# Kernel tuning notes

Measured on AMD Instinct MI355X. Metric: run time of the kernel, lower is better.

Reference implementation:

```python
import jax, jax.numpy as jnp
import numpy as np

NUM_NODES = 100000
NUM_HYPEREDGES = 100000
NNZ = 1600000
K = 64
LAMBDA_ORTHO = 0.1


def setup_inputs() -> dict:
    key = jax.random.key(0)
    k1, k2, k3 = jax.random.split(key, 3)
    Z = jax.random.normal(k1, (NUM_NODES, K), dtype=jnp.float32)
    hyperedge_index = jax.random.randint(k2, (2, NNZ), 0, NUM_HYPEREDGES, dtype=jnp.int64)
    hyperedge_weight = jax.random.uniform(k3, (NUM_HYPEREDGES,), dtype=jnp.float32)
    return {
        "Z": Z,
        "hyperedge_index": hyperedge_index,
        "num_nodes": NUM_NODES,
        "hyperedge_weight": hyperedge_weight,
    }


def reference(Z, hyperedge_index, num_nodes, hyperedge_weight):
    E = hyperedge_weight.shape[0]  # num_hyperedges (static)
    node_idx = hyperedge_index[0]
    edge_idx = hyperedge_index[1]

    # Node degree Dv = sum of incident hyperedge weights; clamp zeros to 1.
    w_exp = hyperedge_weight[edge_idx]                                  # [nnz]
    Dv = jax.ops.segment_sum(w_exp, node_idx, num_segments=num_nodes)   # [N]
    Dv = jnp.where(Dv == 0, jnp.ones_like(Dv), Dv)
    Y = Z * (Dv ** -0.5)[:, None]                                       # [N, k]

    # Hyperedge cardinality De (clamped) and raw counts n_e.
    ones = jnp.ones_like(edge_idx, dtype=Z.dtype)
    n_e = jax.ops.segment_sum(ones, edge_idx, num_segments=E)           # [E]
    De = jnp.where(n_e == 0, jnp.ones_like(n_e), n_e)

    # Closed form for the per-edge pairwise-distance loop:
    # 0.5 * sum_{i,j in e} |y_i - y_j|^2 = n_e * sum_i |y_i|^2 - |sum_i y_i|^2
    Yg = Y[node_idx]                                                    # [nnz, k]
    sum_e = jax.ops.segment_sum(Yg, edge_idx, num_segments=E)           # [E, k]
    ss_e = jax.ops.segment_sum(jnp.sum(Yg * Yg, axis=-1), edge_idx, num_segments=E)  # [E]
    per_edge = n_e * ss_e - jnp.sum(sum_e * sum_e, axis=-1)             # [E]
    loss = jnp.sum(hyperedge_weight / De * per_edge)

    # Orthogonality penalty: ||Y^T Y - I||_F
    k = Z.shape[1]
    G = Y.T @ Y - jnp.eye(k, dtype=Z.dtype)
    ortho_loss = jnp.sqrt(jnp.sum(G * G))

    return loss + LAMBDA_ORTHO * ortho_loss
```

## Files before the change

kernel.cpp:

```cpp
#include <hip/hip_runtime.h>
#include <math.h>

#define NNODES 100000
#define NEDGES 100000
#define NNZV   1600000
#define KDIM   64
#define LAMBDA 0.1f

#define NB    782
#define BSH   7
#define BMASK 127
#define CAP   3072
#define A0B   256
#define A0T   1024
#define CHUNK 6250
#define GMB   512

#define OFF_G       0
#define OFF_PART    16384
#define OFF_ZN      19712
#define OFF_GC1     23040
#define OFF_GC2     26368
#define OFF_S1      29696
#define OFF_S2      9638912
#define OFF_YQ      19248128

#if defined(__has_builtin)
#if __has_builtin(__builtin_amdgcn_cvt_f32_fp8)
#define HAS_CVT_FP8 1
#endif
#if __has_builtin(__builtin_amdgcn_cvt_pk_fp8_f32)
#define HAS_PK_FP8 1
#endif
#if __has_builtin(__builtin_amdgcn_cvt_pk_f32_fp8)
#define HAS_PK_F32_FP8 1
typedef float f32x2 __attribute__((ext_vector_type(2)));
#endif
#endif

__device__ __forceinline__ int load_node(const unsigned* idx, int i, bool i64) {
    return (int)(i64 ? idx[2 * i] : idx[i]);
}
__device__ __forceinline__ int load_edge(const unsigned* idx, int i, bool i64) {
    return (int)(i64 ? idx[2 * (NNZV + i)] : idx[NNZV + i]);
}

__device__ __forceinline__ unsigned char enc_fp8(float x) {
    unsigned u = __float_as_uint(x);
    unsigned s = (u >> 31) << 7;
    unsigned mag = u & 0x7FFFFFFFu;
    if (mag >= 0x43E00000u) return (unsigned char)(s | 0x7Eu);
    if (mag < 0x3C800000u) {
        float a = __uint_as_float(mag);
        int m = (int)rintf(a * 512.0f);
        if (m >= 8) return (unsigned char)(s | 0x08u);
        return (unsigned char)(s | (unsigned)m);
    }
    unsigned lsb = (mag >> 20) & 1u;
    mag += 0x0007FFFFu + lsb;
    unsigned e = (mag >> 23) - 120u;
    return (unsigned char)(s | (e << 3) | ((mag >> 20) & 7u));
}

__device__ __forceinline__ unsigned pack_fp8x4(float y0, float y1, float y2, float y3) {
#ifdef HAS_PK_FP8
    int q = 0;
    q = __builtin_amdgcn_cvt_pk_fp8_f32(y0, y1, q, false);
    q = __builtin_amdgcn_cvt_pk_fp8_f32(y2, y3, q, true);
    return (unsigned)q;
#else
    return (unsigned)enc_fp8(y0) | ((unsigned)enc_fp8(y1) << 8) |
           ((unsigned)enc_fp8(y2) << 16) | ((unsigned)enc_fp8(y3) << 24);
#endif
}

template <int SEL>
__device__ __forceinline__ float dec_fp8(unsigned v) {
#ifdef HAS_CVT_FP8
    return __builtin_amdgcn_cvt_f32_fp8(v, SEL);
#else
    unsigned b = (v >> (8 * SEL)) & 0xFFu;
    unsigned e = (b >> 3) & 15u, m = b & 7u;
    float f = e ? __uint_as_float(((e + 120u) << 23) | (m << 20))
                : (float)m * 0.001953125f;
    return (b & 128u) ? -f : f;
#endif
}

__device__ __forceinline__ void dec4_fp8(unsigned v, float& a0, float& a1,
                                         float& a2, float& a3) {
#ifdef HAS_PK_F32_FP8
    f32x2 lo = __builtin_amdgcn_cvt_pk_f32_fp8((int)v, false);
    f32x2 hi = __builtin_amdgcn_cvt_pk_f32_fp8((int)v, true);
    a0 = lo.x; a1 = lo.y; a2 = hi.x; a3 = hi.y;
#else
    a0 = dec_fp8<0>(v); a1 = dec_fp8<1>(v);
    a2 = dec_fp8<2>(v); a3 = dec_fp8<3>(v);
#endif
}

__global__ void init_kernel(unsigned* __restrict__ gcur1,
                            unsigned* __restrict__ gcur2,
                            float* __restrict__ G) {
    int i = blockIdx.x * 256 + threadIdx.x;
    if (i < NB) {
        gcur1[i] = (unsigned)i * CAP;
        gcur2[i] = (unsigned)i * CAP;
    }
    if (i < KDIM * KDIM) G[i] = 0.0f;
}

__global__ __launch_bounds__(A0T) void sort_kernel(const unsigned* __restrict__ idx,
                                                   unsigned* __restrict__ gcur1,
                                                   unsigned* __restrict__ gcur2,
                                                   unsigned* __restrict__ S1,
                                                   unsigned* __restrict__ S2) {
    __shared__ unsigned stage[CHUNK];
    __shared__ unsigned lhist[NB], lcur[NB], gbase[NB];
    __shared__ unsigned wsum[16], fred[16];
    int which = blockIdx.x >> 8, chunk = blockIdx.x & (A0B - 1);
    int t = threadIdx.x, wave = t >> 6, lane = t & 63;

    unsigned hv = idx[2 * t + 1];
#pragma unroll
    for (int off = 32; off; off >>= 1) hv |= __shfl_xor(hv, off);
    if (lane == 0) fred[wave] = hv;
    for (int j = t; j < NB; j += A0T) lhist[j] = 0u;
    __syncthreads();
    unsigned o = 0;
#pragma unroll
    for (int k = 0; k < 16; ++k) o |= fred[k];
    bool i64 = (o == 0u);

    int base = chunk * CHUNK;
    if (which == 0) {
        for (int i = base + t; i < base + CHUNK; i += A0T)
            atomicAdd(&lhist[load_edge(idx, i, i64) >> BSH], 1u);
    } else {
        for (int i = base + t; i < base + CHUNK; i += A0T)
            atomicAdd(&lhist[load_node(idx, i, i64) >> BSH], 1u);
    }
    __syncthreads();

    unsigned v = (t < NB) ? lhist[t] : 0u;
    unsigned x = v;
#pragma unroll
    for (int off = 1; off < 64; off <<= 1) {
        unsigned y = __shfl_up(x, off);
        if (lane >= off) x += y;
    }
    if (lane == 63) wsum[wave] = x;
    __syncthreads();
    if (t < 16) {
        unsigned a = wsum[t], y = a;
#pragma unroll
        for (int off = 1; off < 16; off <<= 1) {
            unsigned z = __shfl_up(y, off);
            if (t >= off) y += z;
        }
        wsum[t] = y - a;
    }
    __syncthreads();
    if (t < NB) lcur[t] = wsum[wave] + x - v;
    __syncthreads();

    for (int i = base + t; i < base + CHUNK; i += A0T) {
        int node = load_node(idx, i, i64);
        int edge = load_edge(idx, i, i64);
        unsigned key, val;
        if (which == 0) {
            key = (unsigned)edge >> BSH;
            val = (unsigned)node | ((unsigned)(edge & BMASK) << 17);
        } else {
            key = (unsigned)node >> BSH;
            val = (unsigned)edge | ((unsigned)(node & BMASK) << 17);
        }
        unsigned p = atomicAdd(&lcur[key], 1u);
        stage[p] = val;
    }
    __syncthreads();

    unsigned* gcur = which ? gcur2 : gcur1;
    if (t < NB) {
        unsigned c = lhist[t];
        gbase[t] = c ? atomicAdd(&gcur[t], c) : 0u;
    }
    __syncthreads();

    unsigned* S = which ? S2 : S1;
    int li = lane & 7;
    for (int bb = wave * 8 + (lane >> 3); bb < NB; bb += 128) {
        unsigned c = lhist[bb];
        unsigned st = lcur[bb] - c;
        unsigned g = gbase[bb];
        for (unsigned m = li; m < c; m += 8) S[g + m] = stage[st + m];
    }
}

__global__ __launch_bounds__(256) void dvyq_kernel(const unsigned* __restrict__ S2,
                                                   const unsigned* __restrict__ gcur2,
                                                   const float* __restrict__ w,
                                                   const float* __restrict__ Z,
                                                   unsigned* __restrict__ Yq32,
                                                   float* __restrict__ ZN) {
    __shared__ float accd[128];
    __shared__ float red[256];
    int t = threadIdx.x, b = blockIdx.x;
    if (t < 128) accd[t] = 0.0f;
    __syncthreads();
    unsigned cnt = gcur2[b] - (unsigned)b * CAP;
    const unsigned* src = S2 + (size_t)b * CAP;
    for (unsigned i = t; i < cnt; i += 256) {
        unsigned e = src[i];
        atomicAdd(&accd[e >> 17], w[e & 0x1FFFFu]);
    }
    __syncthreads();
    int base = b * 128;
    float zn = 0.0f;
    for (int j = t; j < 128 * 16; j += 256) {
        int row = j >> 4, q = j & 15;
        int node = base + row;
        if (node < NNODES) {
            float4 v = ((const float4*)Z)[node * 16 + q];
            float d = accd[row];
            bool good = d > 0.0f;
            float r = good ? rsqrtf(d) : 1.0f;
            zn += good ? (v.x * v.x + v.y * v.y + v.z * v.z + v.w * v.w) : 0.0f;
            Yq32[node * 16 + q] = pack_fp8x4(v.x * r, v.y * r, v.z * r, v.w * r);
        }
    }
    red[t] = zn;
    __syncthreads();
    for (int s = 128; s > 0; s >>= 1) {
        if (t < s) red[t] += red[t + s];
        __syncthreads();
    }
    if (t == 0) ZN[b] = red[0];
}

__global__ __launch_bounds__(256) void gmat_kernel(const unsigned* __restrict__ Yq32,
                                                   float* __restrict__ G) {
    __shared__ float ys[64][KDIM];
    float acc[16];
#pragma unroll
    for (int i = 0; i < 16; ++i) acc[i] = 0.0f;
    int t = threadIdx.x;
    int c = t & 63;
    int r0 = (t >> 6) * 16;
    for (int base = blockIdx.x * 64; base < NNODES; base += GMB * 64) {
        int rows = min(64, NNODES - base);
        __syncthreads();
        for (int j = t; j < rows * 16; j += 256) {
            unsigned v = Yq32[base * 16 + j];
            int row = j >> 4, q4 = (j & 15) * 4;
            float x0, x1, x2, x3;
            dec4_fp8(v, x0, x1, x2, x3);
            ys[row][q4 + 0] = x0;
            ys[row][q4 + 1] = x1;
            ys[row][q4 + 2] = x2;
            ys[row][q4 + 3] = x3;
        }
        __syncthreads();
#pragma unroll 4
        for (int i = 0; i < rows; ++i) {
            float yc = ys[i][c];
#pragma unroll
            for (int rr = 0; rr < 16; ++rr) acc[rr] += ys[i][r0 + rr] * yc;
        }
    }
#pragma unroll
    for (int rr = 0; rr < 16; ++rr) atomicAdd(&G[(r0 + rr) * KDIM + c], acc[rr]);
}

__global__ __launch_bounds__(512) void bedge_kernel(const unsigned* __restrict__ Yq32,
                                                    const float* __restrict__ w,
                                                    const unsigned* __restrict__ S1,
                                                    const unsigned* __restrict__ gcur1,
                                                    float* __restrict__ part) {
    __shared__ unsigned lhist[128], loffs[128], lcur[128];
    __shared__ unsigned snode[CAP];
    __shared__ float wred[8];
    int t = threadIdx.x, b = blockIdx.x;
    if (t < 128) lhist[t] = 0u;
    __syncthreads();
    unsigned cnt = gcur1[b] - (unsigned)b * CAP;
    const unsigned* src = S1 + (size_t)b * CAP;
    for (unsigned i = t; i < cnt; i += 512)
        atomicAdd(&lhist[src[i] >> 17], 1u);
    __syncthreads();
    if (t < 64) {
        unsigned a = lhist[2 * t], bb = lhist[2 * t + 1];
        unsigned sp = a + bb, x = sp;
#pragma unroll
        for (int off = 1; off < 64; off <<= 1) {
            unsigned y = __shfl_up(x, off);
            if (t >= off) x += y;
        }
        unsigned ex = x - sp;
        loffs[2 * t] = ex;          lcur[2 * t] = ex;
        loffs[2 * t + 1] = ex + a;  lcur[2 * t + 1] = ex + a;
    }
    __syncthreads();
    for (unsigned i = t; i < cnt; i += 512) {
        unsigned e = src[i];
        unsigned pos = atomicAdd(&lcur[e >> 17], 1u);
        snode[pos] = e & 0x1FFFFu;
    }
    __syncthreads();
    int wv = t >> 6, lane = t & 63, ms = lane >> 4, kq = lane & 15;
    float acc = 0.0f;
    for (int el = wv; el < 64; el += 8) {
        int eA = el, eB = el + 64;
        unsigned nA = lhist[eA], nB = lhist[eB];
        if (nA == 0 && nB == 0) continue;
        unsigned begA = loffs[eA], begB = loffs[eB];
        float a0 = 0, a1 = 0, a2 = 0, a3 = 0;
        float c0 = 0, c1 = 0, c2 = 0, c3 = 0;
        unsigned mmax = nA > nB ? nA : nB;
        for (unsigned m = 0; m < mmax; m += 16) {
            unsigned mA0 = m + (unsigned)ms, mA1 = mA0 + 4, mA2 = mA0 + 8, mA3 = mA0 + 12;
            bool oA0 = mA0 < nA, oA1 = mA1 < nA, oA2 = mA2 < nA, oA3 = mA3 < nA;
            bool oB0 = mA0 < nB, oB1 = mA1 < nB, oB2 = mA2 < nB, oB3 = mA3 < nB;
            unsigned nA0 = snode[oA0 ? begA + mA0 : 0];
            unsigned nA1 = snode[oA1 ? begA + mA1 : 0];
            unsigned nA2 = snode[oA2 ? begA + mA2 : 0];
            unsigned nA3 = snode[oA3 ? begA + mA3 : 0];
            unsigned nB0 = snode[oB0 ? begB + mA0 : 0];
            unsigned nB1 = snode[oB1 ? begB + mA1 : 0];
            unsigned nB2 = snode[oB2 ? begB + mA2 : 0];
            unsigned nB3 = snode[oB3 ? begB + mA3 : 0];
            unsigned vA0 = Yq32[nA0 * 16u + (unsigned)kq];
            unsigned vA1 = Yq32[nA1 * 16u + (unsigned)kq];
            unsigned vA2 = Yq32[nA2 * 16u + (unsigned)kq];
            unsigned vA3 = Yq32[nA3 * 16u + (unsigned)kq];
            unsigned vB0 = Yq32[nB0 * 16u + (unsigned)kq];
            unsigned vB1 = Yq32[nB1 * 16u + (unsigned)kq];
            unsigned vB2 = Yq32[nB2 * 16u + (unsigned)kq];
            unsigned vB3 = Yq32[nB3 * 16u + (unsigned)kq];
            float x0, x1, x2, x3;
            dec4_fp8(vA0, x0, x1, x2, x3);
            if (oA0) { a0 += x0; a1 += x1; a2 += x2; a3 += x3; }
            dec4_fp8(vA1, x0, x1, x2, x3);
            if (oA1) { a0 += x0; a1 += x1; a2 += x2; a3 += x3; }
            dec4_fp8(vA2, x0, x1, x2, x3);
            if (oA2) { a0 += x0; a1 += x1; a2 += x2; a3 += x3; }
            dec4_fp8(vA3, x0, x1, x2, x3);
            if (oA3) { a0 += x0; a1 += x1; a2 += x2; a3 += x3; }
            dec4_fp8(vB0, x0, x1, x2, x3);
            if (oB0) { c0 += x0; c1 += x1; c2 += x2; c3 += x3; }
            dec4_fp8(vB1, x0, x1, x2, x3);
            if (oB1) { c0 += x0; c1 += x1; c2 += x2; c3 += x3; }
            dec4_fp8(vB2, x0, x1, x2, x3);
            if (oB2) { c0 += x0; c1 += x1; c2 += x2; c3 += x3; }
            dec4_fp8(vB3, x0, x1, x2, x3);
            if (oB3) { c0 += x0; c1 += x1; c2 += x2; c3 += x3; }
        }
        a0 += __shfl_xor(a0, 16); a0 += __shfl_xor(a0, 32);
        a1 += __shfl_xor(a1, 16); a1 += __shfl_xor(a1, 32);
        a2 += __shfl_xor(a2, 16); a2 += __shfl_xor(a2, 32);
        a3 += __shfl_xor(a3, 16); a3 += __shfl_xor(a3, 32);
        c0 += __shfl_xor(c0, 16); c0 += __shfl_xor(c0, 32);
        c1 += __shfl_xor(c1, 16); c1 += __shfl_xor(c1, 32);
        c2 += __shfl_xor(c2, 16); c2 += __shfl_xor(c2, 32);
        c3 += __shfl_xor(c3, 16); c3 += __shfl_xor(c3, 32);
        float aa = a0 * a0 + a1 * a1 + a2 * a2 + a3 * a3;
        float cc = c0 * c0 + c1 * c1 + c2 * c2 + c3 * c3;
        aa += __shfl_xor(aa, 1); aa += __shfl_xor(aa, 2);
        aa += __shfl_xor(aa, 4); aa += __shfl_xor(aa, 8);
        cc += __shfl_xor(cc, 1); cc += __shfl_xor(cc, 2);
        cc += __shfl_xor(cc, 4); cc += __shfl_xor(cc, 8);
        if (lane == 0) {
            if (nA) acc += (w[b * 128 + eA] / (float)nA) * aa;
            if (nB) acc += (w[b * 128 + eB] / (float)nB) * cc;
        }
    }
    if (lane == 0) wred[wv] = acc;
    __syncthreads();
    if (t == 0) {
        float s = 0.0f;
        for (int i = 0; i < 8; ++i) s += wred[i];
        part[b] = s;
    }
}

__global__ void final_kernel(const float* __restrict__ G,
                             const float* __restrict__ ZN,
                             const float* __restrict__ part,
                             float* __restrict__ out) {
    __shared__ float r1[256], r2[256];
    int t = threadIdx.x;
    float zn = 0.0f, pe = 0.0f, gg = 0.0f;
    for (int i = t; i < NB; i += 256) { zn += ZN[i]; pe += part[i]; }
    for (int i = t; i < KDIM * KDIM; i += 256) {
        int r = i >> 6, c = i & 63;
        float g = G[i] - ((r == c) ? 1.0f : 0.0f);
        gg += g * g;
    }
    r1[t] = zn - pe; r2[t] = gg;
    __syncthreads();
    for (int s = 128; s > 0; s >>= 1) {
        if (t < s) { r1[t] += r1[t + s]; r2[t] += r2[t + s]; }
        __syncthreads();
    }
    if (t == 0) out[0] = r1[0] + LAMBDA * sqrtf(r2[0]);
}

extern "C" void kernel_launch(void* const* d_in, const int* in_sizes, int n_in,
                              void* d_out, int out_size, void* d_ws, size_t ws_size,
                              hipStream_t stream) {
    const float* Z = (const float*)d_in[0];
    const unsigned* idx = (const unsigned*)d_in[1];
    const float* w = (const float*)d_in[3];
    float* out = (float*)d_out;
    char* ws = (char*)d_ws;

    float* G        = (float*)(ws + OFF_G);
    float* part     = (float*)(ws + OFF_PART);
    float* ZN       = (float*)(ws + OFF_ZN);
    unsigned* gcur1 = (unsigned*)(ws + OFF_GC1);
    unsigned* gcur2 = (unsigned*)(ws + OFF_GC2);
    unsigned* S1    = (unsigned*)(ws + OFF_S1);
    unsigned* S2    = (unsigned*)(ws + OFF_S2);
    unsigned* Yq32  = (unsigned*)(ws + OFF_YQ);

    init_kernel<<<16, 256, 0, stream>>>(gcur1, gcur2, G);
    sort_kernel<<<2 * A0B, A0T, 0, stream>>>(idx, gcur1, gcur2, S1, S2);
    dvyq_kernel<<<NB, 256, 0, stream>>>(S2, gcur2, w, Z, Yq32, ZN);
    bedge_kernel<<<NB, 512, 0, stream>>>(Yq32, w, S1, gcur1, part);
    gmat_kernel<<<GMB, 256, 0, stream>>>(Yq32, G);
    final_kernel<<<1, 256, 0, stream>>>(G, ZN, part, out);
}
```

Baseline: 118.2 us.

## Merge Gram-matrix kernel into edge kernel and cache indices in sort registers

The Gram-matrix (Y^T Y) work is folded into the per-edge loss kernel as extra blocks of a single launch, so both run concurrently and one launch is removed. The Gram blocks drop to 256 of 512 threads each, with 8 accumulators per thread. Separately, the sort kernel now loads each chunk's node and edge indices once into registers and reuses them for both the histogram and scatter passes, where it used to read global memory twice. The trade-offs are more registers in sort and a larger shared-memory footprint in the fused kernel, which may lower occupancy for the edge blocks.

```diff
diff --git a/kernel.cpp b/kernel.cpp
--- a/kernel.cpp
+++ b/kernel.cpp
@@ -14,7 +14,7 @@
 #define A0B   256
 #define A0T   1024
 #define CHUNK 6250
-#define GMB   512
+#define GMB   256
 
 #define OFF_G       0
 #define OFF_PART    16384
@@ -133,12 +133,19 @@
     bool i64 = (o == 0u);
 
     int base = chunk * CHUNK;
-    if (which == 0) {
-        for (int i = base + t; i < base + CHUNK; i += A0T)
-            atomicAdd(&lhist[load_edge(idx, i, i64) >> BSH], 1u);
-    } else {
-        for (int i = base + t; i < base + CHUNK; i += A0T)
-            atomicAdd(&lhist[load_node(idx, i, i64) >> BSH], 1u);
+    unsigned nd[7], ed[7];
+#pragma unroll
+    for (int k = 0; k < 7; ++k) {
+        bool ok = (k < 6) || (t < CHUNK - 6 * A0T);
+        int i = base + k * A0T + t;
+        nd[k] = ok ? (unsigned)load_node(idx, i, i64) : 0u;
+        ed[k] = ok ? (unsigned)load_edge(idx, i, i64) : 0u;
+    }
+
+#pragma unroll
+    for (int k = 0; k < 7; ++k) {
+        bool ok = (k < 6) || (t < CHUNK - 6 * A0T);
+        if (ok) atomicAdd(&lhist[(which ? nd[k] : ed[k]) >> BSH], 1u);
     }
     __syncthreads();
 
@@ -164,19 +171,21 @@
     if (t < NB) lcur[t] = wsum[wave] + x - v;
     __syncthreads();
 
-    for (int i = base + t; i < base + CHUNK; i += A0T) {
-        int node = load_node(idx, i, i64);
-        int edge = load_edge(idx, i, i64);
-        unsigned key, val;
-        if (which == 0) {
-            key = (unsigned)edge >> BSH;
-            val = (unsigned)node | ((unsigned)(edge & BMASK) << 17);
-        } else {
-            key = (unsigned)node >> BSH;
-            val = (unsigned)edge | ((unsigned)(node & BMASK) << 17);
-        }
-        unsigned p = atomicAdd(&lcur[key], 1u);
-        stage[p] = val;
+#pragma unroll
+    for (int k = 0; k < 7; ++k) {
+        bool ok = (k < 6) || (t < CHUNK - 6 * A0T);
+        if (ok) {
+            unsigned key, val;
+            if (which == 0) {
+                key = ed[k] >> BSH;
+                val = nd[k] | ((ed[k] & BMASK) << 17);
+            } else {
+                key = nd[k] >> BSH;
+                val = ed[k] | ((nd[k] & BMASK) << 17);
+            }
+            unsigned p = atomicAdd(&lcur[key], 1u);
+            stage[p] = val;
+        }
     }
     __syncthreads();
 
@@ -238,49 +247,51 @@
     if (t == 0) ZN[b] = red[0];
 }
 
-__global__ __launch_bounds__(256) void gmat_kernel(const unsigned* __restrict__ Yq32,
-                                                   float* __restrict__ G) {
-    __shared__ float ys[64][KDIM];
-    float acc[16];
-#pragma unroll
-    for (int i = 0; i < 16; ++i) acc[i] = 0.0f;
-    int t = threadIdx.x;
-    int c = t & 63;
-    int r0 = (t >> 6) * 16;
-    for (int base = blockIdx.x * 64; base < NNODES; base += GMB * 64) {
-        int rows = min(64, NNODES - base);
-        __syncthreads();
-        for (int j = t; j < rows * 16; j += 256) {
-            unsigned v = Yq32[base * 16 + j];
-            int row = j >> 4, q4 = (j & 15) * 4;
-            float x0, x1, x2, x3;
-            dec4_fp8(v, x0, x1, x2, x3);
-            ys[row][q4 + 0] = x0;
-            ys[row][q4 + 1] = x1;
-            ys[row][q4 + 2] = x2;
-            ys[row][q4 + 3] = x3;
-        }
-        __syncthreads();
-#pragma unroll 4
-        for (int i = 0; i < rows; ++i) {
-            float yc = ys[i][c];
-#pragma unroll
-            for (int rr = 0; rr < 16; ++rr) acc[rr] += ys[i][r0 + rr] * yc;
-        }
-    }
-#pragma unroll
-    for (int rr = 0; rr < 16; ++rr) atomicAdd(&G[(r0 + rr) * KDIM + c], acc[rr]);
-}
-
-__global__ __launch_bounds__(512) void bedge_kernel(const unsigned* __restrict__ Yq32,
-                                                    const float* __restrict__ w,
-                                                    const unsigned* __restrict__ S1,
-                                                    const unsigned* __restrict__ gcur1,
-                                                    float* __restrict__ part) {
+__global__ __launch_bounds__(512) void bg_kernel(const unsigned* __restrict__ Yq32,
+                                                 const float* __restrict__ w,
+                                                 const unsigned* __restrict__ S1,
+                                                 const unsigned* __restrict__ gcur1,
+                                                 float* __restrict__ part,
+                                                 float* __restrict__ G) {
     __shared__ unsigned lhist[128], loffs[128], lcur[128];
     __shared__ unsigned snode[CAP];
     __shared__ float wred[8];
+    __shared__ float ys[64][KDIM];
     int t = threadIdx.x, b = blockIdx.x;
+
+    if (b >= NB) {
+        int gb = b - NB;
+        float acc[8];
+#pragma unroll
+        for (int i = 0; i < 8; ++i) acc[i] = 0.0f;
+        int c = t & 63;
+        int r0 = ((t >> 6) & 7) * 8;
+        for (int base = gb * 64; base < NNODES; base += GMB * 64) {
+            int rows = min(64, NNODES - base);
+            __syncthreads();
+            for (int j = t; j < rows * 16; j += 512) {
+                unsigned v = Yq32[base * 16 + j];
+                int row = j >> 4, q4 = (j & 15) * 4;
+                float x0, x1, x2, x3;
+                dec4_fp8(v, x0, x1, x2, x3);
+                ys[row][q4 + 0] = x0;
+                ys[row][q4 + 1] = x1;
+                ys[row][q4 + 2] = x2;
+                ys[row][q4 + 3] = x3;
+            }
+            __syncthreads();
+#pragma unroll 4
+            for (int i = 0; i < rows; ++i) {
+                float yc = ys[i][c];
+#pragma unroll
+                for (int rr = 0; rr < 8; ++rr) acc[rr] += ys[i][r0 + rr] * yc;
+            }
+        }
+#pragma unroll
+        for (int rr = 0; rr < 8; ++rr) atomicAdd(&G[(r0 + rr) * KDIM + c], acc[rr]);
+        return;
+    }
+
     if (t < 128) lhist[t] = 0u;
     __syncthreads();
     unsigned cnt = gcur1[b] - (unsigned)b * CAP;
@@ -426,7 +437,6 @@
     init_kernel<<<16, 256, 0, stream>>>(gcur1, gcur2, G);
     sort_kernel<<<2 * A0B, A0T, 0, stream>>>(idx, gcur1, gcur2, S1, S2);
     dvyq_kernel<<<NB, 256, 0, stream>>>(S2, gcur2, w, Z, Yq32, ZN);
-    bedge_kernel<<<NB, 512, 0, stream>>>(Yq32, w, S1, gcur1, part);
-    gmat_kernel<<<GMB, 256, 0, stream>>>(Yq32, G);
+    bg_kernel<<<NB + GMB, 512, 0, stream>>>(Yq32, w, S1, gcur1, part, G);
     final_kernel<<<1, 256, 0, stream>>>(G, ZN, part, out);
 }
```

After: 107.4 us. 1.1x faster.
